# Kernel optimization log

Measured on AMD Instinct MI355X. Metric: run time of the kernel, lower is better.

The kernel has to match this reference:

```python
import jax, jax.numpy as jnp
import numpy as np

B, N, D, A = 4, 2048, 1024, 256


def setup_inputs() -> dict:
    key = jax.random.key(0)
    k1, k2, k3, k4, k5 = jax.random.split(key, 5)
    s = 1.0 / np.sqrt(D)
    return {
        "inputs": jax.random.normal(k1, (B, N, D), dtype=jnp.float32),
        "attention_mask": jnp.zeros((B, 1, N), dtype=jnp.float32),
        "Wq": jax.random.normal(k2, (D, A), dtype=jnp.float32) * s,
        "bq": jax.random.normal(k3, (A,), dtype=jnp.float32) * 0.01,
        "Wk": jax.random.normal(k4, (D, A), dtype=jnp.float32) * s,
        "bk": jax.random.normal(k5, (A,), dtype=jnp.float32) * 0.01,
    }


def reference(inputs, attention_mask, Wq, bq, Wk, bk):
    # q, k: [B, N, A]; v = inputs: [B, N, D]
    q = jnp.einsum('bnd,da->bna', inputs, Wq) + bq
    k = jnp.einsum('bnd,da->bna', inputs, Wk) + bk
    # unscaled scores, faithful to source (no 1/sqrt(d))
    scores = jnp.einsum('bna,bma->bnm', q, k) + attention_mask  # [B, N, N]
    probs = jax.nn.softmax(scores, axis=-1)
    # dropout is identity in eval mode
    context = jnp.einsum('bnm,bmd->bnd', probs, inputs)  # [B, N, D]
    return context
```

## Files before the change

kernel.cpp:

```cpp
#include <hip/hip_runtime.h>
#include <hip/hip_bf16.h>


#define BB 4
#define NN 2048
#define DD 1024
#define AA 256

using bf16x8 = __attribute__((ext_vector_type(8))) __bf16;
using f32x4  = __attribute__((ext_vector_type(4))) float;

#define MFMA(a, b, c) __builtin_amdgcn_mfma_f32_16x16x32_bf16(a, b, c, 0, 0, 0)

#define VMCNT(n) asm volatile("s_waitcnt vmcnt(" #n ")" ::: "memory")
#define LGKM0()  asm volatile("s_waitcnt lgkmcnt(0)" ::: "memory")
#define SB0()    __builtin_amdgcn_sched_barrier(0)
#define CFENCE() asm volatile("" ::: "memory")
#define BARRIER() __builtin_amdgcn_s_barrier()

static __device__ __forceinline__ unsigned short f2bf(float x) {
    union { float f; unsigned int u; } c; c.f = x;
    unsigned int u = c.u;
    u += 0x7fffu + ((u >> 16) & 1u);
    return (unsigned short)(u >> 16);
}
static __device__ __forceinline__ float bf2f(unsigned short h) {
    union { unsigned int u; float f; } c; c.u = ((unsigned int)h) << 16;
    return c.f;
}

template<int SLOTS>
static __device__ __forceinline__ int swz(int r) {
    return (SLOTS == 4) ? ((r >> 1) & 3) : (r & 7);
}

template<int ROWS, int BK, int THREADS, int I0, int I1>
static __device__ __forceinline__ void stage_part(const unsigned short* __restrict__ g,
                                                  int pitch, unsigned short* lds, int t) {
    constexpr int SLOTS = BK / 8;
#pragma unroll
    for (int i = I0; i < I1; ++i) {
        int tt = t + i * THREADS;
        int row = tt / SLOTS;
        int slot = (tt % SLOTS) ^ swz<SLOTS>(row);
        const char* src = (const char*)(g + (size_t)row * pitch) + slot * 16;
        __builtin_amdgcn_global_load_lds((const unsigned int*)src,
                                         (unsigned int*)((char*)lds + (size_t)tt * 16),
                                         16, 0, 0);
    }
}

template<int BK>
static __device__ __forceinline__ bf16x8 ldsfrag(const unsigned short* lds, int row,
                                                 int ks, int lane) {
    constexpr int SLOTS = BK / 8;
    int r = row + (lane & 15);
    int slot = (ks * 4 + (lane >> 4)) ^ swz<SLOTS>(r);
    return *reinterpret_cast<const bf16x8*>((const char*)lds + (size_t)r * (BK * 2) + slot * 16);
}

__global__ __launch_bounds__(256) void k_prep(const float* __restrict__ X,
                                              unsigned short* __restrict__ Xh,
                                              unsigned short* __restrict__ Xl,
                                              unsigned short* __restrict__ XT) {
    __shared__ unsigned short tile[64][65];
    int t = threadIdx.x;
    int n0 = blockIdx.x * 64, d0 = blockIdx.y * 64;
    const float* Xb = X + (size_t)blockIdx.z * NN * DD;
    unsigned short* Xhb = Xh + (size_t)blockIdx.z * NN * DD;
    unsigned short* Xlb = Xl + (size_t)blockIdx.z * NN * DD;
    unsigned short* XTb = XT + (size_t)blockIdx.z * DD * NN;
    int r = t >> 4, c4 = (t & 15) * 4;
#pragma unroll
    for (int i = 0; i < 4; ++i) {
        int row = r + 16 * i;
        float4 v = *reinterpret_cast<const float4*>(Xb + (size_t)(n0 + row) * DD + d0 + c4);
        ushort4 h, l;
        h.x = f2bf(v.x); l.x = f2bf(v.x - bf2f(h.x));
        h.y = f2bf(v.y); l.y = f2bf(v.y - bf2f(h.y));
        h.z = f2bf(v.z); l.z = f2bf(v.z - bf2f(h.z));
        h.w = f2bf(v.w); l.w = f2bf(v.w - bf2f(h.w));
        *reinterpret_cast<ushort4*>(Xhb + (size_t)(n0 + row) * DD + d0 + c4) = h;
        *reinterpret_cast<ushort4*>(Xlb + (size_t)(n0 + row) * DD + d0 + c4) = l;
        tile[c4 + 0][row] = h.x;
        tile[c4 + 1][row] = h.y;
        tile[c4 + 2][row] = h.z;
        tile[c4 + 3][row] = h.w;
    }
    __syncthreads();
    int j = t & 63, i4 = t >> 6;
#pragma unroll
    for (int jj = i4; jj < 64; jj += 4)
        XTb[(size_t)(d0 + jj) * NN + n0 + j] = tile[jj][j];
}

__global__ __launch_bounds__(256) void k_wsplit(const float* __restrict__ W,
                                                unsigned short* __restrict__ WTh,
                                                unsigned short* __restrict__ WTl) {
    int idx = blockIdx.x * 256 + threadIdx.x;
    int a = idx >> 10;
    int d = idx & (DD - 1);
    float w = W[(size_t)d * AA + a];
    unsigned short hi = f2bf(w);
    WTh[idx] = hi;
    WTl[idx] = f2bf(w - bf2f(hi));
}

__global__ __launch_bounds__(256) void k_proj(const unsigned short* __restrict__ Xh,
                                              const unsigned short* __restrict__ Xl,
                                              const unsigned short* __restrict__ WqTh,
                                              const unsigned short* __restrict__ WqTl,
                                              const unsigned short* __restrict__ WkTh,
                                              const unsigned short* __restrict__ WkTl,
                                              const float* __restrict__ bq,
                                              const float* __restrict__ bk,
                                              unsigned short* __restrict__ Qh,
                                              unsigned short* __restrict__ Ql,
                                              unsigned short* __restrict__ Kh,
                                              unsigned short* __restrict__ Kl) {
    extern __shared__ unsigned short dyn[];
    int t = threadIdx.x, lane = t & 63, wave = t >> 6;
    int bid = blockIdx.x;
    int xcd = bid & 7, idx = bid >> 3;
    int rowpanel = xcd * 16 + (idx >> 2);
    int yy = idx & 3;
    int row0 = rowpanel * 64;
    int which = yy >> 1;
    int col0 = (yy & 1) * 128;
    const unsigned short* BTh = which ? WkTh : WqTh;
    const unsigned short* BTl = which ? WkTl : WqTl;
    const float* bias = which ? bk : bq;
    unsigned short* Oh = which ? Kh : Qh;
    unsigned short* Ol = which ? Kl : Ql;
    const unsigned short* Abase_h = Xh + (size_t)row0 * DD;
    const unsigned short* Abase_l = Xl + (size_t)row0 * DD;
    const unsigned short* Bbase_h = BTh + (size_t)col0 * DD;
    const unsigned short* Bbase_l = BTl + (size_t)col0 * DD;
    int wc = wave * 32;
    f32x4 acc[4][2] = {};
#pragma unroll
    for (int p = 0; p < 2; ++p) {
        unsigned short* bp = dyn + p * 12288;
        int k0 = p * 32;
        stage_part<64, 32, 256, 0, 1>(Abase_h + k0, DD, bp, t);
        stage_part<64, 32, 256, 0, 1>(Abase_l + k0, DD, bp + 2048, t);
        stage_part<128, 32, 256, 0, 2>(Bbase_h + k0, DD, bp + 4096, t);
        stage_part<128, 32, 256, 0, 2>(Bbase_l + k0, DD, bp + 8192, t);
    }
    constexpr int NT = DD / 32;
    int cur = 0;
    for (int tt = 0; tt < NT; ++tt) {
        int st = (cur >= 1) ? cur - 1 : 2;
        CFENCE();
        if (tt == NT - 1) { VMCNT(0); } else { VMCNT(6); }
        BARRIER();
        CFENCE();
        unsigned short* bc = dyn + cur * 12288;
        if (tt + 2 < NT) {
            unsigned short* bs = dyn + st * 12288;
            int k0 = (tt + 2) * 32;
            stage_part<64, 32, 256, 0, 1>(Abase_h + k0, DD, bs, t);
            stage_part<64, 32, 256, 0, 1>(Abase_l + k0, DD, bs + 2048, t);
            stage_part<128, 32, 256, 0, 2>(Bbase_h + k0, DD, bs + 4096, t);
            stage_part<128, 32, 256, 0, 2>(Bbase_l + k0, DD, bs + 8192, t);
        }
        bf16x8 ah[4], al[4], bh[2], bl[2];
#pragma unroll
        for (int f = 0; f < 4; ++f) {
            ah[f] = ldsfrag<32>(bc, f * 16, 0, lane);
            al[f] = ldsfrag<32>(bc + 2048, f * 16, 0, lane);
        }
#pragma unroll
        for (int n = 0; n < 2; ++n) {
            bh[n] = ldsfrag<32>(bc + 4096, wc + n * 16, 0, lane);
            bl[n] = ldsfrag<32>(bc + 8192, wc + n * 16, 0, lane);
        }
        LGKM0();
        SB0();
        __builtin_amdgcn_s_setprio(1);
#pragma unroll
        for (int m = 0; m < 4; ++m)
#pragma unroll
            for (int n = 0; n < 2; ++n) {
                acc[m][n] = MFMA(ah[m], bh[n], acc[m][n]);
                acc[m][n] = MFMA(ah[m], bl[n], acc[m][n]);
                acc[m][n] = MFMA(al[m], bh[n], acc[m][n]);
            }
        __builtin_amdgcn_s_setprio(0);
        cur = (cur == 2) ? 0 : cur + 1;
    }
    int r4 = (lane >> 4) << 2, cl = lane & 15;
#pragma unroll
    for (int m = 0; m < 4; ++m)
#pragma unroll
        for (int n = 0; n < 2; ++n) {
            int col = col0 + wc + n * 16 + cl;
            float bv = bias[col];
#pragma unroll
            for (int r = 0; r < 4; ++r) {
                int row = row0 + m * 16 + r4 + r;
                float v = acc[m][n][r] + bv;
                unsigned short hi = f2bf(v);
                size_t o = (size_t)row * AA + col;
                Oh[o] = hi;
                Ol[o] = f2bf(v - bf2f(hi));
            }
        }
}

__global__ __launch_bounds__(256) void k_scores(const unsigned short* __restrict__ Qh,
                                                const unsigned short* __restrict__ Ql,
                                                const unsigned short* __restrict__ Kh,
                                                const unsigned short* __restrict__ Kl,
                                                float* __restrict__ S) {
    __shared__ unsigned short ldsAh[2][128 * 32], ldsAl[2][128 * 32];
    __shared__ unsigned short ldsBh[2][128 * 32], ldsBl[2][128 * 32];
    int t = threadIdx.x, lane = t & 63, wave = t >> 6;
    int bid = blockIdx.x + 16 * blockIdx.y + 256 * blockIdx.z;
    int sbid = (bid & 7) * 128 + (bid >> 3);
    int b = sbid >> 8;
    int nrow0 = (sbid & 15) * 128;
    int mcol0 = ((sbid >> 4) & 15) * 128;
    const unsigned short* Qhb = Qh + (size_t)(b * NN + nrow0) * AA;
    const unsigned short* Qlb = Ql + (size_t)(b * NN + nrow0) * AA;
    const unsigned short* Khb = Kh + (size_t)(b * NN + mcol0) * AA;
    const unsigned short* Klb = Kl + (size_t)(b * NN + mcol0) * AA;
    int wr = (wave >> 1) * 64, wc = (wave & 1) * 64;
    f32x4 acc[4][4] = {};
    stage_part<128, 32, 256, 0, 2>(Qhb, AA, ldsAh[0], t);
    stage_part<128, 32, 256, 0, 2>(Qlb, AA, ldsAl[0], t);
    stage_part<128, 32, 256, 0, 2>(Khb, AA, ldsBh[0], t);
    stage_part<128, 32, 256, 0, 2>(Klb, AA, ldsBl[0], t);
    constexpr int NT = AA / 32;
    for (int tt = 0; tt < NT; ++tt) {
        int cur = tt & 1;
        CFENCE();
        VMCNT(0);
        BARRIER();
        CFENCE();
        if (tt + 1 < NT) {
            int k0 = (tt + 1) * 32;
            stage_part<128, 32, 256, 0, 2>(Qhb + k0, AA, ldsAh[cur ^ 1], t);
            stage_part<128, 32, 256, 0, 2>(Qlb + k0, AA, ldsAl[cur ^ 1], t);
            stage_part<128, 32, 256, 0, 2>(Khb + k0, AA, ldsBh[cur ^ 1], t);
            stage_part<128, 32, 256, 0, 2>(Klb + k0, AA, ldsBl[cur ^ 1], t);
        }
        bf16x8 ah[4], al[4], bh[4], bl[4];
#pragma unroll
        for (int f = 0; f < 4; ++f) {
            ah[f] = ldsfrag<32>(ldsAh[cur], wr + f * 16, 0, lane);
            al[f] = ldsfrag<32>(ldsAl[cur], wr + f * 16, 0, lane);
            bh[f] = ldsfrag<32>(ldsBh[cur], wc + f * 16, 0, lane);
            bl[f] = ldsfrag<32>(ldsBl[cur], wc + f * 16, 0, lane);
        }
        LGKM0();
        SB0();
        __builtin_amdgcn_s_setprio(1);
#pragma unroll
        for (int m = 0; m < 4; ++m)
#pragma unroll
            for (int n = 0; n < 4; ++n) {
                acc[m][n] = MFMA(ah[m], bh[n], acc[m][n]);
                acc[m][n] = MFMA(ah[m], bl[n], acc[m][n]);
                acc[m][n] = MFMA(al[m], bh[n], acc[m][n]);
            }
        __builtin_amdgcn_s_setprio(0);
    }
    int r4 = (lane >> 4) << 2, cl = lane & 15;
#pragma unroll
    for (int m = 0; m < 4; ++m)
#pragma unroll
        for (int n = 0; n < 4; ++n) {
#pragma unroll
            for (int r = 0; r < 4; ++r) {
                int nrow = nrow0 + wr + m * 16 + r4 + r;
                int mcol = mcol0 + wc + n * 16 + cl;
                S[((size_t)(b * NN + nrow)) * NN + mcol] = acc[m][n][r];
            }
        }
}

__global__ __launch_bounds__(256) void k_softmax(float* __restrict__ S,
                                                 const float* __restrict__ mask) {
    int t = threadIdx.x, lane = t & 63, wave = t >> 6;
    int row = blockIdx.x * 4 + wave;
    int b = row >> 11;
    float* srow = S + (size_t)row * NN;
    const float4* S4 = (const float4*)srow;
    const float4* M4 = (const float4*)(mask + (size_t)b * NN);
    float v[32];
#pragma unroll
    for (int i = 0; i < 8; ++i) {
        float4 s4 = S4[lane + i * 64];
        float4 m4 = M4[lane + i * 64];
        v[4 * i + 0] = s4.x + m4.x;
        v[4 * i + 1] = s4.y + m4.y;
        v[4 * i + 2] = s4.z + m4.z;
        v[4 * i + 3] = s4.w + m4.w;
    }
    float mx = v[0];
#pragma unroll
    for (int i = 1; i < 32; ++i) mx = fmaxf(mx, v[i]);
#pragma unroll
    for (int off = 32; off; off >>= 1) mx = fmaxf(mx, __shfl_xor(mx, off));
    float s = 0.f;
#pragma unroll
    for (int i = 0; i < 32; ++i) { v[i] = __expf(v[i] - mx); s += v[i]; }
#pragma unroll
    for (int off = 32; off; off >>= 1) s += __shfl_xor(s, off);
    float inv = 1.0f / s;
    ushort4* prow4 = (ushort4*)srow;
#pragma unroll
    for (int i = 0; i < 8; ++i) {
        ushort4 w;
        w.x = f2bf(v[4 * i + 0] * inv);
        w.y = f2bf(v[4 * i + 1] * inv);
        w.z = f2bf(v[4 * i + 2] * inv);
        w.w = f2bf(v[4 * i + 3] * inv);
        prow4[lane + i * 64] = w;
    }
}

__global__ __launch_bounds__(512, 2) void k_pv(const float* __restrict__ Sbuf,
                                               const unsigned short* __restrict__ XT,
                                               float* __restrict__ Out) {
    extern __shared__ unsigned short dyn[];
    int t = threadIdx.x, lane = t & 63, wave = t >> 6;
    int wm = wave >> 2, wn = wave & 3;
    int bid = blockIdx.x + 16 * (blockIdx.y + 4 * blockIdx.z);
    int sbid = (bid & 7) * 32 + (bid >> 3);
    int bx = sbid & 15;
    int by = (sbid >> 4) & 3;
    int b = sbid >> 6;
    int nrow0 = bx * 128, d0 = by * 256;
    const unsigned short* Pb = (const unsigned short*)Sbuf + (size_t)(b * NN + nrow0) * (NN * 2);
    const unsigned short* XTb = XT + (size_t)b * DD * NN + (size_t)d0 * NN;
    f32x4 acc[4][4] = {};
    stage_part<128, 64, 512, 0, 2>(Pb, NN * 2, dyn, t);
    stage_part<256, 64, 512, 0, 4>(XTb, NN, dyn + 24576, t);
    stage_part<128, 64, 512, 0, 2>(Pb + 64, NN * 2, dyn + 8192, t);
    stage_part<256, 64, 512, 0, 4>(XTb + 64, NN, dyn + 24576 + 16384, t);
    constexpr int NT = NN / 64;
    int cur = 0;
    for (int kt = 0; kt < NT; ++kt) {
        int st = (cur >= 1) ? cur - 1 : 2;
        CFENCE();
        if (kt == NT - 1) { VMCNT(0); } else { VMCNT(6); }
        BARRIER();
        CFENCE();
        const unsigned short* A  = dyn + cur * 8192;
        const unsigned short* Bt = dyn + 24576 + cur * 16384;
        if (kt + 2 < NT) {
            stage_part<128, 64, 512, 0, 2>(Pb + (kt + 2) * 64, NN * 2, dyn + st * 8192, t);
            stage_part<256, 64, 512, 0, 4>(XTb + (kt + 2) * 64, NN, dyn + 24576 + st * 16384, t);
        }
        bf16x8 pa[4][2], vb[4][2];
#pragma unroll
        for (int mi = 0; mi < 4; ++mi)
#pragma unroll
            for (int ks = 0; ks < 2; ++ks)
                pa[mi][ks] = ldsfrag<64>(A, wm * 64 + mi * 16, ks, lane);
#pragma unroll
        for (int ni = 0; ni < 4; ++ni)
#pragma unroll
            for (int ks = 0; ks < 2; ++ks)
                vb[ni][ks] = ldsfrag<64>(Bt, wn * 64 + ni * 16, ks, lane);
        LGKM0();
        SB0();
        __builtin_amdgcn_s_setprio(1);
#pragma unroll
        for (int ks = 0; ks < 2; ++ks)
#pragma unroll
            for (int mi = 0; mi < 4; ++mi)
#pragma unroll
                for (int ni = 0; ni < 4; ++ni)
                    acc[mi][ni] = MFMA(pa[mi][ks], vb[ni][ks], acc[mi][ni]);
        __builtin_amdgcn_s_setprio(0);
        cur = (cur == 2) ? 0 : cur + 1;
    }
    int r4 = (lane >> 4) << 2, cl = lane & 15;
#pragma unroll
    for (int mi = 0; mi < 4; ++mi)
#pragma unroll
        for (int ni = 0; ni < 4; ++ni) {
#pragma unroll
            for (int r = 0; r < 4; ++r) {
                int row = b * NN + nrow0 + wm * 64 + mi * 16 + r4 + r;
                int dc = d0 + wn * 64 + ni * 16 + cl;
                Out[(size_t)row * DD + dc] = acc[mi][ni][r];
            }
        }
}

extern "C" void kernel_launch(void* const* d_in, const int* in_sizes, int n_in,
                              void* d_out, int out_size, void* d_ws, size_t ws_size,
                              hipStream_t stream) {
    const float* X    = (const float*)d_in[0];
    const float* mask = (const float*)d_in[1];
    const float* Wq   = (const float*)d_in[2];
    const float* bq   = (const float*)d_in[3];
    const float* Wk   = (const float*)d_in[4];
    const float* bk   = (const float*)d_in[5];
    float* Out = (float*)d_out;

    unsigned short* Xh   = (unsigned short*)d_ws;
    unsigned short* Xl   = Xh + (size_t)BB * NN * DD;
    unsigned short* XT   = Xl + (size_t)BB * NN * DD;
    unsigned short* WqTh = XT + (size_t)BB * NN * DD;
    unsigned short* WqTl = WqTh + (size_t)AA * DD;
    unsigned short* WkTh = WqTl + (size_t)AA * DD;
    unsigned short* WkTl = WkTh + (size_t)AA * DD;
    unsigned short* Qh   = WkTl + (size_t)AA * DD;
    unsigned short* Ql   = Qh + (size_t)BB * NN * AA;
    unsigned short* Kh   = Ql + (size_t)BB * NN * AA;
    unsigned short* Kl   = Kh + (size_t)BB * NN * AA;
    float* S = (float*)(Kl + (size_t)BB * NN * AA);

    hipFuncSetAttribute((const void*)k_pv,
                        hipFuncAttributeMaxDynamicSharedMemorySize, 147456);
    hipFuncSetAttribute((const void*)k_proj,
                        hipFuncAttributeMaxDynamicSharedMemorySize, 73728);

    k_prep<<<dim3(NN / 64, DD / 64, BB), 256, 0, stream>>>(X, Xh, Xl, XT);
    k_wsplit<<<dim3((AA * DD) / 256), 256, 0, stream>>>(Wq, WqTh, WqTl);
    k_wsplit<<<dim3((AA * DD) / 256), 256, 0, stream>>>(Wk, WkTh, WkTl);

    k_proj<<<dim3((BB * NN) / 64 * 4), 256, 73728, stream>>>(Xh, Xl, WqTh, WqTl, WkTh, WkTl,
                                                             bq, bk, Qh, Ql, Kh, Kl);

    k_scores<<<dim3(NN / 128, NN / 128, BB), 256, 0, stream>>>(Qh, Ql, Kh, Kl, S);
    k_softmax<<<dim3(BB * NN / 4), 256, 0, stream>>>(S, mask);
    k_pv<<<dim3(16, 4, BB), 512, 147456, stream>>>(S, XT, Out);
}
```

Before: 146.4 us.

## Load P fragments directly into registers and double-buffer only XT in LDS

The PV kernel now reads the probability operand straight from global memory into per-lane MFMA fragments, register double-buffered across iterations, and no longer stages it through shared memory. Only the XT tile is staged in LDS, now with a 2-stage ping-pong instead of a 3-stage ring, which cuts dynamic LDS from 144KB to 64KB. This removes LDS traffic and LDS footprint for P. In exchange, each P load is a strided 16-byte per-lane global read, and the full vmcnt(0) wait plus barrier every half-iteration reduces how far loads can run ahead of compute.

```diff
diff --git a/kernel.cpp b/kernel.cpp
--- a/kernel.cpp
+++ b/kernel.cpp
@@ -333,50 +333,80 @@
     int by = (sbid >> 4) & 3;
     int b = sbid >> 6;
     int nrow0 = bx * 128, d0 = by * 256;
-    const unsigned short* Pb = (const unsigned short*)Sbuf + (size_t)(b * NN + nrow0) * (NN * 2);
+    const unsigned short* P = (const unsigned short*)Sbuf;
+    const unsigned short* paBase =
+        P + (size_t)(b * NN + nrow0 + wm * 64 + (lane & 15)) * (NN * 2) + ((lane >> 4) << 3);
     const unsigned short* XTb = XT + (size_t)b * DD * NN + (size_t)d0 * NN;
     f32x4 acc[4][4] = {};
-    stage_part<128, 64, 512, 0, 2>(Pb, NN * 2, dyn, t);
-    stage_part<256, 64, 512, 0, 4>(XTb, NN, dyn + 24576, t);
-    stage_part<128, 64, 512, 0, 2>(Pb + 64, NN * 2, dyn + 8192, t);
-    stage_part<256, 64, 512, 0, 4>(XTb + 64, NN, dyn + 24576 + 16384, t);
+    bf16x8 paA[4][2], paB[4][2];
+    stage_part<256, 64, 512, 0, 4>(XTb, NN, dyn, t);
+#pragma unroll
+    for (int mi = 0; mi < 4; ++mi)
+#pragma unroll
+        for (int ks = 0; ks < 2; ++ks)
+            paA[mi][ks] = *reinterpret_cast<const bf16x8*>(
+                paBase + (size_t)(mi * 16) * (NN * 2) + ks * 32);
     constexpr int NT = NN / 64;
-    int cur = 0;
-    for (int kt = 0; kt < NT; ++kt) {
-        int st = (cur >= 1) ? cur - 1 : 2;
-        CFENCE();
-        if (kt == NT - 1) { VMCNT(0); } else { VMCNT(6); }
-        BARRIER();
-        CFENCE();
-        const unsigned short* A  = dyn + cur * 8192;
-        const unsigned short* Bt = dyn + 24576 + cur * 16384;
-        if (kt + 2 < NT) {
-            stage_part<128, 64, 512, 0, 2>(Pb + (kt + 2) * 64, NN * 2, dyn + st * 8192, t);
-            stage_part<256, 64, 512, 0, 4>(XTb + (kt + 2) * 64, NN, dyn + 24576 + st * 16384, t);
-        }
-        bf16x8 pa[4][2], vb[4][2];
-#pragma unroll
-        for (int mi = 0; mi < 4; ++mi)
+#pragma unroll 1
+    for (int kt = 0; kt < NT; kt += 2) {
+        {
+            CFENCE(); VMCNT(0); BARRIER(); CFENCE();
+            int kn = kt + 1;
+            stage_part<256, 64, 512, 0, 4>(XTb + kn * 64, NN, dyn + 16384, t);
+#pragma unroll
+            for (int mi = 0; mi < 4; ++mi)
+#pragma unroll
+                for (int ks = 0; ks < 2; ++ks)
+                    paB[mi][ks] = *reinterpret_cast<const bf16x8*>(
+                        paBase + (size_t)(mi * 16) * (NN * 2) + kn * 64 + ks * 32);
+            CFENCE();
+            bf16x8 vb[4][2];
+#pragma unroll
+            for (int ni = 0; ni < 4; ++ni)
+#pragma unroll
+                for (int ks = 0; ks < 2; ++ks)
+                    vb[ni][ks] = ldsfrag<64>(dyn, wn * 64 + ni * 16, ks, lane);
+            LGKM0(); SB0();
+            __builtin_amdgcn_s_setprio(1);
 #pragma unroll
             for (int ks = 0; ks < 2; ++ks)
-                pa[mi][ks] = ldsfrag<64>(A, wm * 64 + mi * 16, ks, lane);
-#pragma unroll
-        for (int ni = 0; ni < 4; ++ni)
+#pragma unroll
+                for (int mi = 0; mi < 4; ++mi)
+#pragma unroll
+                    for (int ni = 0; ni < 4; ++ni)
+                        acc[mi][ni] = MFMA(paA[mi][ks], vb[ni][ks], acc[mi][ni]);
+            __builtin_amdgcn_s_setprio(0);
+        }
+        {
+            CFENCE(); VMCNT(0); BARRIER(); CFENCE();
+            int kn = kt + 2;
+            if (kn < NT) {
+                stage_part<256, 64, 512, 0, 4>(XTb + kn * 64, NN, dyn, t);
+#pragma unroll
+                for (int mi = 0; mi < 4; ++mi)
+#pragma unroll
+                    for (int ks = 0; ks < 2; ++ks)
+                        paA[mi][ks] = *reinterpret_cast<const bf16x8*>(
+                            paBase + (size_t)(mi * 16) * (NN * 2) + kn * 64 + ks * 32);
+            }
+            CFENCE();
+            bf16x8 vb[4][2];
+#pragma unroll
+            for (int ni = 0; ni < 4; ++ni)
+#pragma unroll
+                for (int ks = 0; ks < 2; ++ks)
+                    vb[ni][ks] = ldsfrag<64>(dyn + 16384, wn * 64 + ni * 16, ks, lane);
+            LGKM0(); SB0();
+            __builtin_amdgcn_s_setprio(1);
 #pragma unroll
             for (int ks = 0; ks < 2; ++ks)
-                vb[ni][ks] = ldsfrag<64>(Bt, wn * 64 + ni * 16, ks, lane);
-        LGKM0();
-        SB0();
-        __builtin_amdgcn_s_setprio(1);
-#pragma unroll
-        for (int ks = 0; ks < 2; ++ks)
-#pragma unroll
-            for (int mi = 0; mi < 4; ++mi)
-#pragma unroll
-                for (int ni = 0; ni < 4; ++ni)
-                    acc[mi][ni] = MFMA(pa[mi][ks], vb[ni][ks], acc[mi][ni]);
-        __builtin_amdgcn_s_setprio(0);
-        cur = (cur == 2) ? 0 : cur + 1;
+#pragma unroll
+                for (int mi = 0; mi < 4; ++mi)
+#pragma unroll
+                    for (int ni = 0; ni < 4; ++ni)
+                        acc[mi][ni] = MFMA(paB[mi][ks], vb[ni][ks], acc[mi][ni]);
+            __builtin_amdgcn_s_setprio(0);
+        }
     }
     int r4 = (lane >> 4) << 2, cl = lane & 15;
 #pragma unroll
@@ -417,7 +447,7 @@
     float* S = (float*)(Kl + (size_t)BB * NN * AA);
 
     hipFuncSetAttribute((const void*)k_pv,
-                        hipFuncAttributeMaxDynamicSharedMemorySize, 147456);
+                        hipFuncAttributeMaxDynamicSharedMemorySize, 65536);
     hipFuncSetAttribute((const void*)k_proj,
                         hipFuncAttributeMaxDynamicSharedMemorySize, 73728);
 
@@ -430,5 +460,5 @@
 
     k_scores<<<dim3(NN / 128, NN / 128, BB), 256, 0, stream>>>(Qh, Ql, Kh, Kl, S);
     k_softmax<<<dim3(BB * NN / 4), 256, 0, stream>>>(S, mask);
-    k_pv<<<dim3(16, 4, BB), 512, 147456, stream>>>(S, XT, Out);
-}
+    k_pv<<<dim3(16, 4, BB), 512, 65536, stream>>>(S, XT, Out);
+}
```

Measured after the change: 193.5 us. 32.1% more time.

## Split PV main loop into two k-halves with interleaved prefetch and LDS reads

Applied to the files above, without the earlier changes.

Restructures the P·V GEMM inner loop into two phases, one per k-substep. Each phase issues its own LDS fragment reads, then a portion of the global-to-LDS prefetch for tile kt+2, followed by barriers and 16 MFMAs. The goal is to spread global-load issue across the MFMA work and cut register pressure by holding only half the fragments at once. The cost is extra barriers per iteration, which may add synchronisation stalls.

```diff
diff --git a/kernel.cpp b/kernel.cpp
--- a/kernel.cpp
+++ b/kernel.cpp
@@ -350,32 +350,60 @@
         CFENCE();
         const unsigned short* A  = dyn + cur * 8192;
         const unsigned short* Bt = dyn + 24576 + cur * 16384;
-        if (kt + 2 < NT) {
-            stage_part<128, 64, 512, 0, 2>(Pb + (kt + 2) * 64, NN * 2, dyn + st * 8192, t);
-            stage_part<256, 64, 512, 0, 4>(XTb + (kt + 2) * 64, NN, dyn + 24576 + st * 16384, t);
-        }
-        bf16x8 pa[4][2], vb[4][2];
-#pragma unroll
-        for (int mi = 0; mi < 4; ++mi)
-#pragma unroll
-            for (int ks = 0; ks < 2; ++ks)
-                pa[mi][ks] = ldsfrag<64>(A, wm * 64 + mi * 16, ks, lane);
-#pragma unroll
-        for (int ni = 0; ni < 4; ++ni)
-#pragma unroll
-            for (int ks = 0; ks < 2; ++ks)
-                vb[ni][ks] = ldsfrag<64>(Bt, wn * 64 + ni * 16, ks, lane);
-        LGKM0();
-        SB0();
-        __builtin_amdgcn_s_setprio(1);
-#pragma unroll
-        for (int ks = 0; ks < 2; ++ks)
+        unsigned short* As = dyn + st * 8192;
+        unsigned short* Bs = dyn + 24576 + st * 16384;
+        const unsigned short* Pn = Pb + (kt + 2) * 64;
+        const unsigned short* Bn = XTb + (kt + 2) * 64;
+        bool pf = (kt + 2 < NT);
+        {
+            bf16x8 pa[4], vb[4];
 #pragma unroll
             for (int mi = 0; mi < 4; ++mi)
+                pa[mi] = ldsfrag<64>(A, wm * 64 + mi * 16, 0, lane);
+#pragma unroll
+            for (int ni = 0; ni < 4; ++ni)
+                vb[ni] = ldsfrag<64>(Bt, wn * 64 + ni * 16, 0, lane);
+            if (pf) {
+                stage_part<128, 64, 512, 0, 2>(Pn, NN * 2, As, t);
+                stage_part<256, 64, 512, 0, 1>(Bn, NN, Bs, t);
+            }
+            CFENCE();
+            BARRIER();
+            LGKM0();
+            SB0();
+            __builtin_amdgcn_s_setprio(1);
+#pragma unroll
+            for (int mi = 0; mi < 4; ++mi)
 #pragma unroll
                 for (int ni = 0; ni < 4; ++ni)
-                    acc[mi][ni] = MFMA(pa[mi][ks], vb[ni][ks], acc[mi][ni]);
-        __builtin_amdgcn_s_setprio(0);
+                    acc[mi][ni] = MFMA(pa[mi], vb[ni], acc[mi][ni]);
+            __builtin_amdgcn_s_setprio(0);
+            CFENCE();
+            BARRIER();
+        }
+        {
+            bf16x8 pa[4], vb[4];
+#pragma unroll
+            for (int mi = 0; mi < 4; ++mi)
+                pa[mi] = ldsfrag<64>(A, wm * 64 + mi * 16, 1, lane);
+#pragma unroll
+            for (int ni = 0; ni < 4; ++ni)
+                vb[ni] = ldsfrag<64>(Bt, wn * 64 + ni * 16, 1, lane);
+            if (pf) {
+                stage_part<256, 64, 512, 1, 4>(Bn, NN, Bs, t);
+            }
+            CFENCE();
+            BARRIER();
+            LGKM0();
+            SB0();
+            __builtin_amdgcn_s_setprio(1);
+#pragma unroll
+            for (int mi = 0; mi < 4; ++mi)
+#pragma unroll
+                for (int ni = 0; ni < 4; ++ni)
+                    acc[mi][ni] = MFMA(pa[mi], vb[ni], acc[mi][ni]);
+            __builtin_amdgcn_s_setprio(0);
+        }
         cur = (cur == 2) ? 0 : cur + 1;
     }
     int r4 = (lane >> 4) << 2, cl = lane & 15;
```

Result: no change. 147.5 us (+0.7%).
